# Kernel tuning notes

Hardware: AMD Instinct MI355X
Metric: run time of the kernel (lower is better)

## Reference

```python
import jax, jax.numpy as jnp
import numpy as np

B, T, V, C, NB, NOPS = 8, 2048, 4096, 128, 64, 8

_NONLIN = [
    lambda h: h,
    jax.nn.relu,
    lambda h: jax.nn.gelu(h, approximate=False),
    lambda h: jnp.square(h),
    lambda h: -h,
    jnp.abs,
    jnp.tanh,
    jax.nn.sigmoid,
]


def setup_inputs() -> dict:
    key = jax.random.key(0)
    ks = jax.random.split(key, 6)
    s = 0.02
    return {
        "x": jax.random.normal(ks[0], (B, T, V), dtype=jnp.float32),
        "basis": jax.random.normal(ks[1], (V, 2 * NB), dtype=jnp.float32),
        "read_coeffs": jax.random.normal(ks[2], (C, 2 * NB), dtype=jnp.float32) * s,
        "write_coeffs": jax.random.normal(ks[3], (C, 2 * NB), dtype=jnp.float32) * s,
        "op_logits": jnp.zeros((NOPS,), dtype=jnp.float32),
        "op_weights": jax.random.normal(ks[4], (NOPS, C, C), dtype=jnp.float32) * s,
        "op_biases": jnp.zeros((NOPS, C), dtype=jnp.float32),
        "out_scale": jnp.float32(0.1),
    }


def op_bank(values, op_logits, op_weights, op_biases):
    # values: (B, T, C); soft mixture of 8 small channel transforms
    w = jax.nn.softmax(op_logits)  # (n_ops,)
    result = jnp.zeros_like(values)
    for i in range(NOPS):
        h = values @ op_weights[i] + op_biases[i]
        h = _NONLIN[i % len(_NONLIN)](h)
        result = result + w[i] * h
    return result


def reference(x, basis, read_coeffs, write_coeffs, op_logits, op_weights, op_biases, out_scale):
    # READ: Fourier soft addressing over V registers, normalized over registers (axis 0)
    read_w = jax.nn.softmax(basis @ read_coeffs.T, axis=0)  # (V, C)
    values = x @ read_w  # (B, T, C)
    # SELECT OP + APPLY
    values = op_bank(values, op_logits, op_weights, op_biases)
    # WRITE: unnormalized Fourier addressing back to registers
    write_w = basis @ write_coeffs.T  # (V, C)
    return (values @ write_w.T) * out_scale  # (B, T, V)
```

## Files before the change

kernel.cpp:

```cpp
#include <hip/hip_runtime.h>
#include <math.h>

#define M_TOT 16384
#define V_DIM 4096
#define C_DIM 128

typedef __bf16 bf16;
typedef __bf16 bf16x8 __attribute__((ext_vector_type(8)));
typedef float f32x4 __attribute__((ext_vector_type(4)));

__device__ inline f32x4 zero4() { f32x4 z; z[0]=0.f; z[1]=0.f; z[2]=0.f; z[3]=0.f; return z; }

__device__ inline bf16 f2bf(float f) {
  union { float f; unsigned u; } a; a.f = f;
  unsigned r = (a.u + 0x7FFFu + ((a.u >> 16) & 1u)) >> 16;
  union { unsigned short s; bf16 b; } o; o.s = (unsigned short)r;
  return o.b;
}

__device__ inline bf16x8 cvt8(float4 a, float4 b) {
  bf16x8 r;
  r[0]=f2bf(a.x); r[1]=f2bf(a.y); r[2]=f2bf(a.z); r[3]=f2bf(a.w);
  r[4]=f2bf(b.x); r[5]=f2bf(b.y); r[6]=f2bf(b.z); r[7]=f2bf(b.w);
  return r;
}

__global__ __launch_bounds__(256) void k_logits(const float* __restrict__ basis,
                                                const float* __restrict__ rc,
                                                float* __restrict__ LT) {
  __shared__ __align__(16) bf16 Asm[128][136];
  __shared__ __align__(16) bf16 Bsm[128][136];
  const int t = threadIdx.x;
  const int v0 = blockIdx.x * 128;
  const int lane = t & 63, wave = t >> 6, fm = lane & 15, quad = lane >> 4;

  {
    const int row = t >> 1, c0 = (t & 1) * 64;
    const float4* p = (const float4*)(rc + row * 128 + c0);
    bf16x8* d = (bf16x8*)&Asm[row][c0];
#pragma unroll
    for (int j = 0; j < 8; j++) { float4 a = p[2*j], b = p[2*j+1]; d[j] = cvt8(a, b); }
  }
  {
    const int row = t >> 1, c0 = (t & 1) * 64;
    const float4* p = (const float4*)(basis + (size_t)(v0 + row) * 128 + c0);
    bf16x8* d = (bf16x8*)&Bsm[row][c0];
#pragma unroll
    for (int j = 0; j < 8; j++) { float4 a = p[2*j], b = p[2*j+1]; d[j] = cvt8(a, b); }
  }
  __syncthreads();

  f32x4 acc[2][8];
#pragma unroll
  for (int m = 0; m < 2; m++)
#pragma unroll
    for (int n = 0; n < 8; n++) acc[m][n] = zero4();

#pragma unroll
  for (int kk = 0; kk < 4; kk++) {
    bf16x8 af[2];
#pragma unroll
    for (int m = 0; m < 2; m++)
      af[m] = *(const bf16x8*)&Asm[wave * 32 + m * 16 + fm][kk * 32 + quad * 8];
#pragma unroll
    for (int nt = 0; nt < 8; nt++) {
      bf16x8 bfr = *(const bf16x8*)&Bsm[nt * 16 + fm][kk * 32 + quad * 8];
#pragma unroll
      for (int m = 0; m < 2; m++)
        acc[m][nt] = __builtin_amdgcn_mfma_f32_16x16x32_bf16(af[m], bfr, acc[m][nt], 0, 0, 0);
    }
  }
#pragma unroll
  for (int m = 0; m < 2; m++)
#pragma unroll
    for (int nt = 0; nt < 8; nt++)
#pragma unroll
      for (int r = 0; r < 4; r++) {
        int c = wave * 32 + m * 16 + quad * 4 + r;
        LT[(size_t)c * V_DIM + v0 + nt * 16 + fm] = acc[m][nt][r];
      }
}

__global__ __launch_bounds__(256) void k_softmax(const float* __restrict__ LT,
                                                 bf16* __restrict__ RT) {
  const int c = blockIdx.x, t = threadIdx.x;
  __shared__ float red[256];
  const float* row = LT + (size_t)c * V_DIM;
  float e[16];
  float lmax = -3.0e38f;
#pragma unroll
  for (int j = 0; j < 16; j++) { e[j] = row[t + 256 * j]; lmax = fmaxf(lmax, e[j]); }
  red[t] = lmax;
  __syncthreads();
  for (int off = 128; off > 0; off >>= 1) {
    if (t < off) red[t] = fmaxf(red[t], red[t + off]);
    __syncthreads();
  }
  const float gmax = red[0];
  __syncthreads();
  float lsum = 0.f;
#pragma unroll
  for (int j = 0; j < 16; j++) { e[j] = __expf(e[j] - gmax); lsum += e[j]; }
  red[t] = lsum;
  __syncthreads();
  for (int off = 128; off > 0; off >>= 1) {
    if (t < off) red[t] += red[t + off];
    __syncthreads();
  }
  const float inv = 1.f / red[0];
#pragma unroll
  for (int j = 0; j < 16; j++)
    RT[(size_t)c * V_DIM + t + 256 * j] = f2bf(e[j] * inv);
}

__global__ __launch_bounds__(256) void k_w2(const float* __restrict__ basis,
                                            const float* __restrict__ wc,
                                            bf16* __restrict__ W2) {
  __shared__ __align__(16) bf16 Asm[64][136];
  __shared__ __align__(16) bf16 Bsm[128][136];
  const int t = threadIdx.x;
  const int v0 = blockIdx.x * 64;
  const int lane = t & 63, wave = t >> 6, fm = lane & 15, quad = lane >> 4;

  {
    const int row = t >> 2, c0 = (t & 3) * 32;
    const float4* p = (const float4*)(basis + (size_t)(v0 + row) * 128 + c0);
    bf16x8* d = (bf16x8*)&Asm[row][c0];
#pragma unroll
    for (int j = 0; j < 4; j++) { float4 a = p[2*j], b = p[2*j+1]; d[j] = cvt8(a, b); }
  }
  {
    const int row = t >> 1, c0 = (t & 1) * 64;
    const float4* p = (const float4*)(wc + row * 128 + c0);
    bf16x8* d = (bf16x8*)&Bsm[row][c0];
#pragma unroll
    for (int j = 0; j < 8; j++) { float4 a = p[2*j], b = p[2*j+1]; d[j] = cvt8(a, b); }
  }
  __syncthreads();

  f32x4 acc[8];
#pragma unroll
  for (int n = 0; n < 8; n++) acc[n] = zero4();
#pragma unroll
  for (int kk = 0; kk < 4; kk++) {
    bf16x8 af = *(const bf16x8*)&Asm[wave * 16 + fm][kk * 32 + quad * 8];
#pragma unroll
    for (int nt = 0; nt < 8; nt++) {
      bf16x8 bfr = *(const bf16x8*)&Bsm[nt * 16 + fm][kk * 32 + quad * 8];
      acc[nt] = __builtin_amdgcn_mfma_f32_16x16x32_bf16(af, bfr, acc[nt], 0, 0, 0);
    }
  }
#pragma unroll
  for (int nt = 0; nt < 8; nt++)
#pragma unroll
    for (int r = 0; r < 4; r++) {
      int v = v0 + wave * 16 + quad * 4 + r;
      W2[v * 128 + nt * 16 + fm] = f2bf(acc[nt][r]);
    }
}

__global__ __launch_bounds__(256) void k_ops(const float* __restrict__ opw,
                                             bf16* __restrict__ WTO) {
  int idx = blockIdx.x * 256 + threadIdx.x;
  int i = idx >> 14, rem = idx & 16383, n = rem >> 7, k = rem & 127;
  WTO[idx] = f2bf(opw[(i << 14) + k * 128 + n]);
}

__global__ __launch_bounds__(256) void k_gemm1(const float* __restrict__ x,
                                               const bf16* __restrict__ RT,
                                               bf16* __restrict__ PART) {
  __shared__ __align__(16) bf16 Asm[64][72];
  __shared__ __align__(16) bf16 Bsm[128][72];
  const int t = threadIdx.x;
  const int kc = blockIdx.x & 3;
  const int m0 = (blockIdx.x >> 2) * 64;
  const int lane = t & 63, wave = t >> 6;
  const int fm = lane & 15, quad = lane >> 4;

  f32x4 acc[8];
#pragma unroll
  for (int i = 0; i < 8; i++) acc[i] = zero4();

  const int ar = t >> 2, ac = (t & 3) * 16;
  const int br = t >> 1, bc = (t & 1) * 32;
  const float* xp = x + (size_t)(m0 + ar) * V_DIM + ac;
  const bf16* bp = RT + (size_t)br * V_DIM + bc;
  const int kbeg = kc * 1024, kend = kbeg + 1024;

  for (int k0 = kbeg; k0 < kend; k0 += 64) {
    float4 a0 = *(const float4*)(xp + k0);
    float4 a1 = *(const float4*)(xp + k0 + 4);
    float4 a2 = *(const float4*)(xp + k0 + 8);
    float4 a3 = *(const float4*)(xp + k0 + 12);
    uint4 b0 = *(const uint4*)(bp + k0);
    uint4 b1 = *(const uint4*)(bp + k0 + 8);
    uint4 b2 = *(const uint4*)(bp + k0 + 16);
    uint4 b3 = *(const uint4*)(bp + k0 + 24);
    __syncthreads();
    *(bf16x8*)&Asm[ar][ac]     = cvt8(a0, a1);
    *(bf16x8*)&Asm[ar][ac + 8] = cvt8(a2, a3);
    *(uint4*)&Bsm[br][bc]      = b0;
    *(uint4*)&Bsm[br][bc + 8]  = b1;
    *(uint4*)&Bsm[br][bc + 16] = b2;
    *(uint4*)&Bsm[br][bc + 24] = b3;
    __syncthreads();
    bf16x8 af0 = *(const bf16x8*)&Asm[wave * 16 + fm][quad * 8];
    bf16x8 af1 = *(const bf16x8*)&Asm[wave * 16 + fm][32 + quad * 8];
#pragma unroll
    for (int nt = 0; nt < 8; nt++) {
      bf16x8 bf0 = *(const bf16x8*)&Bsm[nt * 16 + fm][quad * 8];
      bf16x8 bf1 = *(const bf16x8*)&Bsm[nt * 16 + fm][32 + quad * 8];
      acc[nt] = __builtin_amdgcn_mfma_f32_16x16x32_bf16(af0, bf0, acc[nt], 0, 0, 0);
      acc[nt] = __builtin_amdgcn_mfma_f32_16x16x32_bf16(af1, bf1, acc[nt], 0, 0, 0);
    }
  }
  bf16* po = PART + (size_t)kc * (M_TOT * C_DIM);
#pragma unroll
  for (int nt = 0; nt < 8; nt++)
#pragma unroll
    for (int r = 0; r < 4; r++) {
      int row = m0 + wave * 16 + quad * 4 + r;
      po[row * 128 + nt * 16 + fm] = f2bf(acc[nt][r]);
    }
}

__device__ inline float apply_nonlin(int i, float v) {
  switch (i) {
    case 0: return v;
    case 1: return fmaxf(v, 0.f);
    case 2: return 0.5f * v * (1.f + erff(v * 0.70710678118654752f));
    case 3: return v * v;
    case 4: return -v;
    case 5: return fabsf(v);
    case 6: return tanhf(v);
    default: return 1.f / (1.f + __expf(-v));
  }
}

__global__ __launch_bounds__(256) void k_opbank(const bf16* __restrict__ PART,
                                                const bf16* __restrict__ WTO,
                                                const float* __restrict__ op_logits,
                                                const float* __restrict__ op_biases,
                                                bf16* __restrict__ val2) {
  __shared__ __align__(16) bf16 Asm[32][136];
  __shared__ __align__(16) bf16 Bsm[128][136];
  const int t = threadIdx.x;
  const int m0 = blockIdx.x * 32;
  const int lane = t & 63, wave = t >> 6;
  const int fm = lane & 15, quad = lane >> 4;
  const int mf = wave & 1, nh = wave >> 1;

  float w[8];
  {
    float lm = -3.0e38f;
#pragma unroll
    for (int i = 0; i < 8; i++) { w[i] = op_logits[i]; lm = fmaxf(lm, w[i]); }
    float s = 0.f;
#pragma unroll
    for (int i = 0; i < 8; i++) { w[i] = __expf(w[i] - lm); s += w[i]; }
    float inv = 1.f / s;
#pragma unroll
    for (int i = 0; i < 8; i++) w[i] *= inv;
  }

  {
    const int row = t >> 3, c0 = (t & 7) * 16;
    float accA[16];
#pragma unroll
    for (int j = 0; j < 16; j++) accA[j] = 0.f;
#pragma unroll
    for (int p = 0; p < 4; p++) {
      const bf16x8* q = (const bf16x8*)(PART + (size_t)p * (M_TOT * C_DIM) + (m0 + row) * 128 + c0);
      bf16x8 u0 = q[0], u1 = q[1];
#pragma unroll
      for (int j = 0; j < 8; j++) { accA[j] += (float)u0[j]; accA[8 + j] += (float)u1[j]; }
    }
    bf16x8 o0, o1;
#pragma unroll
    for (int j = 0; j < 8; j++) { o0[j] = f2bf(accA[j]); o1[j] = f2bf(accA[8 + j]); }
    *(bf16x8*)&Asm[row][c0] = o0;
    *(bf16x8*)&Asm[row][c0 + 8] = o1;
  }
  __syncthreads();

  bf16x8 af[4];
#pragma unroll
  for (int kk = 0; kk < 4; kk++)
    af[kk] = *(const bf16x8*)&Asm[mf * 16 + fm][kk * 32 + quad * 8];

  f32x4 res[4];
#pragma unroll
  for (int j = 0; j < 4; j++) res[j] = zero4();

  const int brow = t >> 1, boff = (t & 1) * 64;
  for (int i = 0; i < 8; i++) {
    __syncthreads();
    {
      const uint4* p = (const uint4*)(WTO + i * 16384 + brow * 128 + boff);
      uint4* d = (uint4*)&Bsm[brow][boff];
#pragma unroll
      for (int j = 0; j < 8; j++) d[j] = p[j];
    }
    __syncthreads();
#pragma unroll
    for (int j = 0; j < 4; j++) {
      const int nt = nh * 4 + j;
      f32x4 h = zero4();
#pragma unroll
      for (int kk = 0; kk < 4; kk++) {
        bf16x8 bfr = *(const bf16x8*)&Bsm[nt * 16 + fm][kk * 32 + quad * 8];
        h = __builtin_amdgcn_mfma_f32_16x16x32_bf16(af[kk], bfr, h, 0, 0, 0);
      }
      float bias = op_biases[i * 128 + nt * 16 + fm];
#pragma unroll
      for (int r = 0; r < 4; r++) {
        float vv = h[r] + bias;
        res[j][r] += w[i] * apply_nonlin(i, vv);
      }
    }
  }
#pragma unroll
  for (int j = 0; j < 4; j++) {
    const int nt = nh * 4 + j;
#pragma unroll
    for (int r = 0; r < 4; r++) {
      int row = m0 + mf * 16 + quad * 4 + r;
      val2[row * 128 + nt * 16 + fm] = f2bf(res[j][r]);
    }
  }
}

struct G2S { bf16 A[64][136]; bf16 B[128][136]; };
union G2U { G2S s; float C[64][132]; };

__global__ __launch_bounds__(256) void k_gemm2(const bf16* __restrict__ val2,
                                               const bf16* __restrict__ W2,
                                               const float* __restrict__ p_scale,
                                               float* __restrict__ out) {
  __shared__ __align__(16) G2U u;
  const int t = threadIdx.x;
  const int n0 = (blockIdx.x >> 8) * 128;
  const int m0 = (blockIdx.x & 255) * 64;
  const int lane = t & 63, wave = t >> 6;
  const int fm = lane & 15, quad = lane >> 4;

  {
    const int row = t >> 2, off = (t & 3) * 32;
    const uint4* p = (const uint4*)(val2 + (m0 + row) * 128 + off);
    uint4* d = (uint4*)&u.s.A[row][off];
#pragma unroll
    for (int j = 0; j < 4; j++) d[j] = p[j];
  }
  {
    const int row = t >> 1, off = (t & 1) * 64;
    const uint4* p = (const uint4*)(W2 + (n0 + row) * 128 + off);
    uint4* d = (uint4*)&u.s.B[row][off];
#pragma unroll
    for (int j = 0; j < 8; j++) d[j] = p[j];
  }
  __syncthreads();

  const float scale = *p_scale;
  bf16x8 af[4];
#pragma unroll
  for (int kk = 0; kk < 4; kk++)
    af[kk] = *(const bf16x8*)&u.s.A[wave * 16 + fm][kk * 32 + quad * 8];

  f32x4 acc[8];
#pragma unroll
  for (int nt = 0; nt < 8; nt++) {
    acc[nt] = zero4();
#pragma unroll
    for (int kk = 0; kk < 4; kk++) {
      bf16x8 bfr = *(const bf16x8*)&u.s.B[nt * 16 + fm][kk * 32 + quad * 8];
      acc[nt] = __builtin_amdgcn_mfma_f32_16x16x32_bf16(af[kk], bfr, acc[nt], 0, 0, 0);
    }
  }
  __syncthreads();
#pragma unroll
  for (int nt = 0; nt < 8; nt++)
#pragma unroll
    for (int r = 0; r < 4; r++)
      u.C[wave * 16 + quad * 4 + r][nt * 16 + fm] = acc[nt][r] * scale;
  __syncthreads();
#pragma unroll
  for (int j = 0; j < 8; j++) {
    int idx = t + 256 * j;
    int row = idx >> 5, c4 = idx & 31;
    float4 v = *(const float4*)&u.C[row][c4 * 4];
    *(float4*)(out + (size_t)(m0 + row) * V_DIM + n0 + c4 * 4) = v;
  }
}

extern "C" void kernel_launch(void* const* d_in, const int* in_sizes, int n_in,
                              void* d_out, int out_size, void* d_ws, size_t ws_size,
                              hipStream_t stream) {
  const float* x      = (const float*)d_in[0];
  const float* basis  = (const float*)d_in[1];
  const float* rc     = (const float*)d_in[2];
  const float* wc     = (const float*)d_in[3];
  const float* oplog  = (const float*)d_in[4];
  const float* opw    = (const float*)d_in[5];
  const float* opb    = (const float*)d_in[6];
  const float* oscale = (const float*)d_in[7];
  float* out = (float*)d_out;
  char* ws = (char*)d_ws;

  float* LT  = (float*)(ws);
  bf16* RT   = (bf16*)(ws + 2097152);
  bf16* W2   = (bf16*)(ws + 3145728);
  bf16* WTO  = (bf16*)(ws + 4194304);
  bf16* PART = (bf16*)(ws + 4456448);
  bf16* VAL2 = (bf16*)(ws + 21233664);

  k_logits <<<V_DIM / 128, 256, 0, stream>>>(basis, rc, LT);
  k_w2     <<<V_DIM / 64, 256, 0, stream>>>(basis, wc, W2);
  k_ops    <<<512, 256, 0, stream>>>(opw, WTO);
  k_softmax<<<C_DIM, 256, 0, stream>>>(LT, RT);
  k_gemm1  <<<(M_TOT / 64) * 4, 256, 0, stream>>>(x, RT, PART);
  k_opbank <<<M_TOT / 32, 256, 0, stream>>>(PART, WTO, oplog, opb, VAL2);
  k_gemm2  <<<(M_TOT / 64) * (V_DIM / 128), 256, 0, stream>>>(VAL2, W2, oscale, out);
}
```

Measured before the change: 581.1 us.

## Double-buffer gemm1 with direct global-to-LDS loads and merge prep kernels

Rewrites the first GEMM to double-buffer the read-weight tile in LDS using global_load_lds with an XOR swizzle. The x operand now goes straight from global memory into registers and is converted to bf16 there, with no LDS staging. Loads for the next K step are issued before computing the current one, to hide memory latency over the dominant 256MB read of x. The three small preparation kernels are also merged into one launch to cut launch overhead. The cost is extra register pressure from the prefetched float4s, and the swizzle indexing has to be exactly right.

Result: no change. 577.3 us (-0.7%).

```diff
diff --git a/kernel.cpp b/kernel.cpp
--- a/kernel.cpp
+++ b/kernel.cpp
@@ -25,60 +25,117 @@
   return r;
 }
 
-__global__ __launch_bounds__(256) void k_logits(const float* __restrict__ basis,
-                                                const float* __restrict__ rc,
-                                                float* __restrict__ LT) {
-  __shared__ __align__(16) bf16 Asm[128][136];
-  __shared__ __align__(16) bf16 Bsm[128][136];
+__device__ inline void gld_lds16(const void* g, void* l) {
+  __builtin_amdgcn_global_load_lds((const __attribute__((address_space(1))) void*)g,
+                                   (__attribute__((address_space(3))) void*)l, 16, 0, 0);
+}
+
+union PrepU {
+  struct { bf16 A[128][136]; bf16 B[128][136]; } lg;
+  struct { bf16 A[64][136];  bf16 B[128][136]; } w2;
+};
+
+__global__ __launch_bounds__(256) void k_prep(const float* __restrict__ basis,
+                                              const float* __restrict__ rc,
+                                              const float* __restrict__ wc,
+                                              const float* __restrict__ opw,
+                                              float* __restrict__ LT,
+                                              bf16* __restrict__ W2,
+                                              bf16* __restrict__ WTO) {
+  __shared__ __align__(16) PrepU pu;
   const int t = threadIdx.x;
-  const int v0 = blockIdx.x * 128;
+  const int bid = blockIdx.x;
   const int lane = t & 63, wave = t >> 6, fm = lane & 15, quad = lane >> 4;
 
-  {
-    const int row = t >> 1, c0 = (t & 1) * 64;
-    const float4* p = (const float4*)(rc + row * 128 + c0);
-    bf16x8* d = (bf16x8*)&Asm[row][c0];
-#pragma unroll
-    for (int j = 0; j < 8; j++) { float4 a = p[2*j], b = p[2*j+1]; d[j] = cvt8(a, b); }
-  }
-  {
-    const int row = t >> 1, c0 = (t & 1) * 64;
-    const float4* p = (const float4*)(basis + (size_t)(v0 + row) * 128 + c0);
-    bf16x8* d = (bf16x8*)&Bsm[row][c0];
-#pragma unroll
-    for (int j = 0; j < 8; j++) { float4 a = p[2*j], b = p[2*j+1]; d[j] = cvt8(a, b); }
-  }
-  __syncthreads();
-
-  f32x4 acc[2][8];
-#pragma unroll
-  for (int m = 0; m < 2; m++)
-#pragma unroll
-    for (int n = 0; n < 8; n++) acc[m][n] = zero4();
-
-#pragma unroll
-  for (int kk = 0; kk < 4; kk++) {
-    bf16x8 af[2];
+  if (bid < 32) {
+    const int v0 = bid * 128;
+    {
+      const int row = t >> 1, c0 = (t & 1) * 64;
+      const float4* p = (const float4*)(rc + row * 128 + c0);
+      bf16x8* d = (bf16x8*)&pu.lg.A[row][c0];
+#pragma unroll
+      for (int j = 0; j < 8; j++) { float4 a = p[2*j], b = p[2*j+1]; d[j] = cvt8(a, b); }
+    }
+    {
+      const int row = t >> 1, c0 = (t & 1) * 64;
+      const float4* p = (const float4*)(basis + (size_t)(v0 + row) * 128 + c0);
+      bf16x8* d = (bf16x8*)&pu.lg.B[row][c0];
+#pragma unroll
+      for (int j = 0; j < 8; j++) { float4 a = p[2*j], b = p[2*j+1]; d[j] = cvt8(a, b); }
+    }
+    __syncthreads();
+
+    f32x4 acc[2][8];
 #pragma unroll
     for (int m = 0; m < 2; m++)
-      af[m] = *(const bf16x8*)&Asm[wave * 32 + m * 16 + fm][kk * 32 + quad * 8];
-#pragma unroll
-    for (int nt = 0; nt < 8; nt++) {
-      bf16x8 bfr = *(const bf16x8*)&Bsm[nt * 16 + fm][kk * 32 + quad * 8];
+#pragma unroll
+      for (int n = 0; n < 8; n++) acc[m][n] = zero4();
+
+#pragma unroll
+    for (int kk = 0; kk < 4; kk++) {
+      bf16x8 af[2];
 #pragma unroll
       for (int m = 0; m < 2; m++)
-        acc[m][nt] = __builtin_amdgcn_mfma_f32_16x16x32_bf16(af[m], bfr, acc[m][nt], 0, 0, 0);
-    }
-  }
-#pragma unroll
-  for (int m = 0; m < 2; m++)
+        af[m] = *(const bf16x8*)&pu.lg.A[wave * 32 + m * 16 + fm][kk * 32 + quad * 8];
+#pragma unroll
+      for (int nt = 0; nt < 8; nt++) {
+        bf16x8 bfr = *(const bf16x8*)&pu.lg.B[nt * 16 + fm][kk * 32 + quad * 8];
+#pragma unroll
+        for (int m = 0; m < 2; m++)
+          acc[m][nt] = __builtin_amdgcn_mfma_f32_16x16x32_bf16(af[m], bfr, acc[m][nt], 0, 0, 0);
+      }
+    }
+#pragma unroll
+    for (int m = 0; m < 2; m++)
+#pragma unroll
+      for (int nt = 0; nt < 8; nt++)
+#pragma unroll
+        for (int r = 0; r < 4; r++) {
+          int c = wave * 32 + m * 16 + quad * 4 + r;
+          LT[(size_t)c * V_DIM + v0 + nt * 16 + fm] = acc[m][nt][r];
+        }
+  } else if (bid < 96) {
+    const int v0 = (bid - 32) * 64;
+    {
+      const int row = t >> 2, c0 = (t & 3) * 32;
+      const float4* p = (const float4*)(basis + (size_t)(v0 + row) * 128 + c0);
+      bf16x8* d = (bf16x8*)&pu.w2.A[row][c0];
+#pragma unroll
+      for (int j = 0; j < 4; j++) { float4 a = p[2*j], b = p[2*j+1]; d[j] = cvt8(a, b); }
+    }
+    {
+      const int row = t >> 1, c0 = (t & 1) * 64;
+      const float4* p = (const float4*)(wc + row * 128 + c0);
+      bf16x8* d = (bf16x8*)&pu.w2.B[row][c0];
+#pragma unroll
+      for (int j = 0; j < 8; j++) { float4 a = p[2*j], b = p[2*j+1]; d[j] = cvt8(a, b); }
+    }
+    __syncthreads();
+
+    f32x4 acc[8];
+#pragma unroll
+    for (int n = 0; n < 8; n++) acc[n] = zero4();
+#pragma unroll
+    for (int kk = 0; kk < 4; kk++) {
+      bf16x8 af = *(const bf16x8*)&pu.w2.A[wave * 16 + fm][kk * 32 + quad * 8];
+#pragma unroll
+      for (int nt = 0; nt < 8; nt++) {
+        bf16x8 bfr = *(const bf16x8*)&pu.w2.B[nt * 16 + fm][kk * 32 + quad * 8];
+        acc[nt] = __builtin_amdgcn_mfma_f32_16x16x32_bf16(af, bfr, acc[nt], 0, 0, 0);
+      }
+    }
 #pragma unroll
     for (int nt = 0; nt < 8; nt++)
 #pragma unroll
       for (int r = 0; r < 4; r++) {
-        int c = wave * 32 + m * 16 + quad * 4 + r;
-        LT[(size_t)c * V_DIM + v0 + nt * 16 + fm] = acc[m][nt][r];
+        int v = v0 + wave * 16 + quad * 4 + r;
+        W2[v * 128 + nt * 16 + fm] = f2bf(acc[nt][r]);
       }
+  } else {
+    int idx = (bid - 96) * 256 + t;
+    int i = idx >> 14, rem = idx & 16383, n = rem >> 7, k = rem & 127;
+    WTO[idx] = f2bf(opw[(i << 14) + k * 128 + n]);
+  }
 }
 
 __global__ __launch_bounds__(256) void k_softmax(const float* __restrict__ LT,
@@ -113,107 +170,83 @@
     RT[(size_t)c * V_DIM + t + 256 * j] = f2bf(e[j] * inv);
 }
 
-__global__ __launch_bounds__(256) void k_w2(const float* __restrict__ basis,
-                                            const float* __restrict__ wc,
-                                            bf16* __restrict__ W2) {
-  __shared__ __align__(16) bf16 Asm[64][136];
-  __shared__ __align__(16) bf16 Bsm[128][136];
-  const int t = threadIdx.x;
-  const int v0 = blockIdx.x * 64;
-  const int lane = t & 63, wave = t >> 6, fm = lane & 15, quad = lane >> 4;
-
-  {
-    const int row = t >> 2, c0 = (t & 3) * 32;
-    const float4* p = (const float4*)(basis + (size_t)(v0 + row) * 128 + c0);
-    bf16x8* d = (bf16x8*)&Asm[row][c0];
-#pragma unroll
-    for (int j = 0; j < 4; j++) { float4 a = p[2*j], b = p[2*j+1]; d[j] = cvt8(a, b); }
-  }
-  {
-    const int row = t >> 1, c0 = (t & 1) * 64;
-    const float4* p = (const float4*)(wc + row * 128 + c0);
-    bf16x8* d = (bf16x8*)&Bsm[row][c0];
-#pragma unroll
-    for (int j = 0; j < 8; j++) { float4 a = p[2*j], b = p[2*j+1]; d[j] = cvt8(a, b); }
-  }
-  __syncthreads();
-
-  f32x4 acc[8];
-#pragma unroll
-  for (int n = 0; n < 8; n++) acc[n] = zero4();
-#pragma unroll
-  for (int kk = 0; kk < 4; kk++) {
-    bf16x8 af = *(const bf16x8*)&Asm[wave * 16 + fm][kk * 32 + quad * 8];
-#pragma unroll
-    for (int nt = 0; nt < 8; nt++) {
-      bf16x8 bfr = *(const bf16x8*)&Bsm[nt * 16 + fm][kk * 32 + quad * 8];
-      acc[nt] = __builtin_amdgcn_mfma_f32_16x16x32_bf16(af, bfr, acc[nt], 0, 0, 0);
-    }
-  }
-#pragma unroll
-  for (int nt = 0; nt < 8; nt++)
-#pragma unroll
-    for (int r = 0; r < 4; r++) {
-      int v = v0 + wave * 16 + quad * 4 + r;
-      W2[v * 128 + nt * 16 + fm] = f2bf(acc[nt][r]);
-    }
-}
-
-__global__ __launch_bounds__(256) void k_ops(const float* __restrict__ opw,
-                                             bf16* __restrict__ WTO) {
-  int idx = blockIdx.x * 256 + threadIdx.x;
-  int i = idx >> 14, rem = idx & 16383, n = rem >> 7, k = rem & 127;
-  WTO[idx] = f2bf(opw[(i << 14) + k * 128 + n]);
-}
-
-__global__ __launch_bounds__(256) void k_gemm1(const float* __restrict__ x,
-                                               const bf16* __restrict__ RT,
-                                               bf16* __restrict__ PART) {
-  __shared__ __align__(16) bf16 Asm[64][72];
-  __shared__ __align__(16) bf16 Bsm[128][72];
+__global__ __launch_bounds__(256, 4) void k_gemm1(const float* __restrict__ x,
+                                                  const bf16* __restrict__ RT,
+                                                  bf16* __restrict__ PART) {
+  __shared__ __align__(16) bf16 Bsm[2][128][64];
   const int t = threadIdx.x;
   const int kc = blockIdx.x & 3;
   const int m0 = (blockIdx.x >> 2) * 64;
   const int lane = t & 63, wave = t >> 6;
   const int fm = lane & 15, quad = lane >> 4;
+  const int sw = (fm & 7) << 4;
+
+  const int c_row = wave * 32 + (lane >> 3);
+  const int src_colbyte = ((lane & 7) * 16) ^ ((lane >> 3) << 4);
+  const bf16* bp = RT + (size_t)c_row * V_DIM + (src_colbyte >> 1);
+
+  const float* xp = x + (size_t)(m0 + wave * 16 + fm) * V_DIM + quad * 8;
 
   f32x4 acc[8];
 #pragma unroll
   for (int i = 0; i < 8; i++) acc[i] = zero4();
 
-  const int ar = t >> 2, ac = (t & 3) * 16;
-  const int br = t >> 1, bc = (t & 1) * 32;
-  const float* xp = x + (size_t)(m0 + ar) * V_DIM + ac;
-  const bf16* bp = RT + (size_t)br * V_DIM + bc;
-  const int kbeg = kc * 1024, kend = kbeg + 1024;
-
-  for (int k0 = kbeg; k0 < kend; k0 += 64) {
-    float4 a0 = *(const float4*)(xp + k0);
-    float4 a1 = *(const float4*)(xp + k0 + 4);
-    float4 a2 = *(const float4*)(xp + k0 + 8);
-    float4 a3 = *(const float4*)(xp + k0 + 12);
-    uint4 b0 = *(const uint4*)(bp + k0);
-    uint4 b1 = *(const uint4*)(bp + k0 + 8);
-    uint4 b2 = *(const uint4*)(bp + k0 + 16);
-    uint4 b3 = *(const uint4*)(bp + k0 + 24);
-    __syncthreads();
-    *(bf16x8*)&Asm[ar][ac]     = cvt8(a0, a1);
-    *(bf16x8*)&Asm[ar][ac + 8] = cvt8(a2, a3);
-    *(uint4*)&Bsm[br][bc]      = b0;
-    *(uint4*)&Bsm[br][bc + 8]  = b1;
-    *(uint4*)&Bsm[br][bc + 16] = b2;
-    *(uint4*)&Bsm[br][bc + 24] = b3;
-    __syncthreads();
-    bf16x8 af0 = *(const bf16x8*)&Asm[wave * 16 + fm][quad * 8];
-    bf16x8 af1 = *(const bf16x8*)&Asm[wave * 16 + fm][32 + quad * 8];
-#pragma unroll
-    for (int nt = 0; nt < 8; nt++) {
-      bf16x8 bf0 = *(const bf16x8*)&Bsm[nt * 16 + fm][quad * 8];
-      bf16x8 bf1 = *(const bf16x8*)&Bsm[nt * 16 + fm][32 + quad * 8];
-      acc[nt] = __builtin_amdgcn_mfma_f32_16x16x32_bf16(af0, bf0, acc[nt], 0, 0, 0);
-      acc[nt] = __builtin_amdgcn_mfma_f32_16x16x32_bf16(af1, bf1, acc[nt], 0, 0, 0);
-    }
-  }
+  const int kbeg = kc * 1024;
+
+#define G1_ISSUE_B(buf, koff)                                                  \
+  {                                                                            \
+    _Pragma("unroll")                                                          \
+    for (int jj = 0; jj < 4; jj++)                                             \
+      gld_lds16(bp + (size_t)jj * 8 * V_DIM + (koff),                          \
+                (char*)&Bsm[buf][0][0] + (wave * 4 + jj) * 1024);              \
+  }
+
+#define G1_ISSUE_A(p0, p1, p2, p3, koff)                                       \
+  {                                                                            \
+    p0 = *(const float4*)(xp + (koff));                                        \
+    p1 = *(const float4*)(xp + (koff) + 4);                                    \
+    p2 = *(const float4*)(xp + (koff) + 32);                                   \
+    p3 = *(const float4*)(xp + (koff) + 36);                                   \
+  }
+
+#define G1_COMPUTE(buf, p0, p1, p2, p3)                                        \
+  {                                                                            \
+    bf16x8 af0 = cvt8(p0, p1);                                                 \
+    bf16x8 af1 = cvt8(p2, p3);                                                 \
+    const char* bb = (const char*)&Bsm[buf][0][0];                             \
+    _Pragma("unroll")                                                          \
+    for (int nt = 0; nt < 8; nt++) {                                           \
+      const char* rp = bb + (nt * 16 + fm) * 128;                              \
+      bf16x8 b0 = *(const bf16x8*)(rp + ((quad * 16) ^ sw));                   \
+      bf16x8 b1 = *(const bf16x8*)(rp + ((64 + quad * 16) ^ sw));              \
+      acc[nt] = __builtin_amdgcn_mfma_f32_16x16x32_bf16(af0, b0, acc[nt], 0, 0, 0); \
+      acc[nt] = __builtin_amdgcn_mfma_f32_16x16x32_bf16(af1, b1, acc[nt], 0, 0, 0); \
+    }                                                                          \
+  }
+
+  float4 aE0, aE1, aE2, aE3, aO0, aO1, aO2, aO3;
+
+  G1_ISSUE_B(0, kbeg);
+  G1_ISSUE_A(aE0, aE1, aE2, aE3, kbeg);
+
+#pragma unroll
+  for (int s = 0; s < 8; s++) {
+    const int k0 = kbeg + s * 128;
+    __syncthreads();
+    G1_ISSUE_B(1, k0 + 64);
+    G1_ISSUE_A(aO0, aO1, aO2, aO3, k0 + 64);
+    G1_COMPUTE(0, aE0, aE1, aE2, aE3);
+    __syncthreads();
+    if (s < 7) {
+      G1_ISSUE_B(0, k0 + 128);
+      G1_ISSUE_A(aE0, aE1, aE2, aE3, k0 + 128);
+    }
+    G1_COMPUTE(1, aO0, aO1, aO2, aO3);
+  }
+#undef G1_ISSUE_B
+#undef G1_ISSUE_A
+#undef G1_COMPUTE
+
   bf16* po = PART + (size_t)kc * (M_TOT * C_DIM);
 #pragma unroll
   for (int nt = 0; nt < 8; nt++)
@@ -413,9 +446,7 @@
   bf16* PART = (bf16*)(ws + 4456448);
   bf16* VAL2 = (bf16*)(ws + 21233664);
 
-  k_logits <<<V_DIM / 128, 256, 0, stream>>>(basis, rc, LT);
-  k_w2     <<<V_DIM / 64, 256, 0, stream>>>(basis, wc, W2);
-  k_ops    <<<512, 256, 0, stream>>>(opw, WTO);
+  k_prep   <<<608, 256, 0, stream>>>(basis, rc, wc, opw, LT, W2, WTO);
   k_softmax<<<C_DIM, 256, 0, stream>>>(LT, RT);
   k_gemm1  <<<(M_TOT / 64) * 4, 256, 0, stream>>>(x, RT, PART);
   k_opbank <<<M_TOT / 32, 256, 0, stream>>>(PART, WTO, oplog, opb, VAL2);
```
